# Performance work log

Measured on AMD Instinct MI355X. Metric: run time of the kernel, lower is better.

Reference implementation:

```python
import jax, jax.numpy as jnp
import numpy as np

N = 768        # nodes
F = 64         # invariant (0e) hidden channels
V = 16         # vector (1e) hidden channels
NB = 8         # bessel basis size
HR = 64        # radial MLP hidden
T = 2          # interactions
RO_S = 32      # invariant readout channels
RO_V = 16      # vector readout channels
RMAX = 10.0
AVG = float(N - 1)   # avg_num_neighbors (fully connected)
P = F + V + F + V + V  # tensor-product paths: s*Y0->0e, dot(v,Y1)->0e, s*Y1->1e, v*Y0->1e, cross(v,Y1)->1e


def _edges(n):
    # fully connected neighbor list (cut_off = 1e6, no pbc): all i != j
    s, r = np.meshgrid(np.arange(n), np.arange(n), indexing='ij')
    m = s != r
    return jnp.asarray(s[m]), jnp.asarray(r[m])


def _bessel(r):
    # bessel_basis(number=NB): sqrt(2/r_max) * sin(n*pi*r/r_max) / r
    n = jnp.arange(1, NB + 1, dtype=r.dtype)
    return jnp.sqrt(2.0 / RMAX) * jnp.sin(n * jnp.pi * r[:, None] / RMAX) / r[:, None]


def _envelope(r):
    # soft_envelope: 1.2 * sus(2*(1 - r/r_max)), sus(u) = exp(-1/u) for u>0 else 0
    u = 2.0 * (1.0 - r / RMAX)
    safe = jnp.where(u > 0, u, 1.0)
    return 1.2 * jnp.where(u > 0, jnp.exp(-1.0 / safe), 0.0)


def setup_inputs() -> dict:
    key = jax.random.key(0)
    ks = jax.random.split(key, 12)
    rn = lambda k, shp, fan: jax.random.normal(k, shp, jnp.float32) / np.sqrt(fan)
    return {
        'x': jax.random.normal(ks[0], (N, 3), jnp.float32),
        'embed': rn(ks[1], (1, F), 1),
        'w_node_s': rn(ks[2], (T, F, F), F),
        'w_node_v': rn(ks[3], (T, V, V), V),
        'w_rad1': rn(ks[4], (T, NB, HR), NB),
        'b_rad1': jnp.zeros((T, HR), jnp.float32),
        'w_rad2': rn(ks[5], (T, HR, P), HR),
        'w_mix_s': rn(ks[6], (T, F + V, F), F + V),
        'w_mix_v': rn(ks[7], (T, F + 2 * V, V), F + 2 * V),
        'w_gate': rn(ks[8], (T, F, V), F),
        'w_ro_s': rn(ks[9], (T, F, RO_S), F),
        'w_ro_v': rn(ks[10], (T, V, RO_V), V),
    }


def reference(x, embed, w_node_s, w_node_v, w_rad1, b_rad1, w_rad2,
              w_mix_s, w_mix_v, w_gate, w_ro_s, w_ro_v):
    n = x.shape[0]
    com = jnp.mean(x, axis=-2)                       # [3] centre of mass
    senders, receivers = _edges(n)
    vec = x[receivers] - x[senders]                  # [E,3] edge relative vectors
    r = jnp.linalg.norm(vec, axis=-1)                # [E]
    rhat = vec / r[:, None]                          # Y1 spherical harmonics (l=1)
    rb = _bessel(r)                                  # [E,NB]
    env = _envelope(r)                               # [E]

    h_s = jnp.broadcast_to(embed[0], (n, F))         # species embedding (all species 0)
    h_v = jnp.zeros((n, V, 3), x.dtype)
    out_s = jnp.zeros((n, RO_S), x.dtype)
    out_v = jnp.zeros((n, RO_V, 3), x.dtype)

    for t in range(T):
        # node-wise linear before gather
        hs = h_s @ w_node_s[t]                                    # [N,F]
        hv = jnp.einsum('nvc,vw->nwc', h_v, w_node_v[t])          # [N,V,3]
        es = hs[senders]                                          # [E,F]
        ev = hv[senders]                                          # [E,V,3]
        # per-edge tensor-product path weights from radial MLP, enveloped
        R = jax.nn.silu(rb @ w_rad1[t] + b_rad1[t]) @ w_rad2[t] * env[:, None]  # [E,P]
        r1, r2, r3, r4, r5 = (R[:, :F], R[:, F:F + V], R[:, F + V:2 * F + V],
                              R[:, 2 * F + V:2 * F + 2 * V], R[:, 2 * F + 2 * V:])
        # equivariant tensor products with Y0=1, Y1=rhat
        dot = jnp.einsum('evc,ec->ev', ev, rhat)                  # 1e x 1e -> 0e
        msg_s = jnp.concatenate([es * r1, dot * r2], axis=-1)     # [E,F+V]
        v1 = (es * r3)[:, :, None] * rhat[:, None, :]             # 0e x 1e -> 1e  [E,F,3]
        v2 = ev * r4[:, :, None]                                  # 1e x 0e -> 1e  [E,V,3]
        v3 = jnp.cross(ev, rhat[:, None, :]) * r5[:, :, None]     # 1e x 1e -> 1e  [E,V,3]
        msg_v = jnp.concatenate([v1, v2, v3], axis=1)             # [E,F+2V,3]
        # scatter-aggregate to receivers
        agg_s = jax.ops.segment_sum(msg_s, receivers, num_segments=n) / AVG
        agg_v = jax.ops.segment_sum(msg_v, receivers, num_segments=n) / AVG
        # mix + gated nonlinearity
        m_s = agg_s @ w_mix_s[t]                                  # [N,F]
        m_v = jnp.einsum('npc,pv->nvc', agg_v, w_mix_v[t])        # [N,V,3]
        h_s = jax.nn.silu(m_s)
        gate = jax.nn.sigmoid(m_s @ w_gate[t])                    # [N,V]
        h_v = gate[:, :, None] * m_v
        # readout (summed over interactions)
        out_s = out_s + h_s @ w_ro_s[t]
        out_v = out_v + jnp.einsum('nvc,vk->nkc', h_v, w_ro_v[t])

    return out_s, out_v + com
```

## Files before the change

### kernel.cpp

```cpp
#include <hip/hip_runtime.h>
#include <hip/hip_bf16.h>
#include <math.h>

#define Nn 768
#define Ff 64
#define Vv 16
#define NBb 8
#define HRr 64
#define Pp 176
#define TBL 2048
#define ROWC 192
#define RMAXF 10.0f
#define AVGF 767.0f
#define SCALE 204.8f

#define WS_COM   0
#define WS_ES0   16
#define WS_XP    128
#define WS_HST   4096
#define WS_HVT   53248
#define WS_OS    102400
#define WS_OV    126976
#define WS_AGG   163840
#define WS_TBL   458752
#define AGGSTRIDE 368

__device__ __forceinline__ unsigned short f2bf(float f) {
  unsigned b = __float_as_uint(f);
  return (unsigned short)((b + 0x7fffu + ((b >> 16) & 1u)) >> 16);
}
__device__ __forceinline__ float lp(unsigned u, float f) {
  float a = __uint_as_float(u << 16);
  float b = __uint_as_float(u & 0xffff0000u);
  return fmaf(f, b - a, a);
}

__global__ void k_pre(const float* __restrict__ x, const float* __restrict__ embed,
                      const float* __restrict__ wns, float* __restrict__ ws) {
  int b = blockIdx.x, tid = threadIdx.x;
  if (b == 0) {
    __shared__ float red[256][3];
    float a0 = 0, a1 = 0, a2 = 0;
    for (int n = tid; n < Nn; n += 256) {
      a0 += x[n * 3 + 0]; a1 += x[n * 3 + 1]; a2 += x[n * 3 + 2];
    }
    red[tid][0] = a0; red[tid][1] = a1; red[tid][2] = a2;
    __syncthreads();
    if (tid < 3) {
      float a = 0;
      for (int k = 0; k < 256; ++k) a += red[k][tid];
      ws[WS_COM + tid] = a * (1.0f / Nn);
    }
  } else if (b == 1) {
    for (int n = tid; n < Nn; n += 256) {
      ws[WS_XP + n * 4 + 0] = x[n * 3 + 0];
      ws[WS_XP + n * 4 + 1] = x[n * 3 + 1];
      ws[WS_XP + n * 4 + 2] = x[n * 3 + 2];
      ws[WS_XP + n * 4 + 3] = 0.0f;
    }
  } else {
    if (tid < 64) {
      float a = 0;
      for (int k = 0; k < 64; ++k) a = fmaf(embed[k], wns[k * 64 + tid], a);
      ws[WS_ES0 + tid] = a;
    }
  }
}

__global__ __launch_bounds__(256) void k_table(const float* __restrict__ w1,
                                               const float* __restrict__ b1,
                                               const float* __restrict__ w2,
                                               float* __restrict__ ws, int t) {
  __shared__ float w2s[64][Pp];
  __shared__ float w1s[NBb][64];
  __shared__ float b1s[64];
  __shared__ float hid[9][65];
  const int tid = threadIdx.x;
  const int r0 = blockIdx.x * 8;
  const float* W2 = w2 + t * HRr * Pp;
  for (int k = tid; k < 64 * Pp; k += 256) w2s[k / Pp][k % Pp] = W2[k];
  for (int k = tid; k < NBb * 64; k += 256) w1s[k >> 6][k & 63] = w1[t * NBb * 64 + k];
  if (tid < 64) b1s[tid] = b1[t * 64 + tid];
  __syncthreads();
  {
    int rl4 = tid >> 6, h = tid & 63;
    const float c0 = 0.447213595f;
    const float pif = 3.14159265358979f;
    for (int pass = 0; pass < 3; ++pass) {
      int row_l = pass * 4 + rl4;
      if (row_l < 9) {
        int row = r0 + row_l;
        float r = row * (RMAXF / TBL);
        float acc = b1s[h];
        if (row == 0) {
          for (int n = 0; n < NBb; ++n) acc = fmaf(c0 * (n + 1) * (pif / RMAXF), w1s[n][h], acc);
        } else {
          float inv = 1.0f / r;
          for (int n = 0; n < NBb; ++n)
            acc = fmaf(c0 * sinf((n + 1) * pif * r / RMAXF) * inv, w1s[n][h], acc);
        }
        hid[row_l][h] = acc / (1.0f + expf(-acc));
      }
    }
  }
  __syncthreads();
  unsigned* T = (unsigned*)(ws + WS_TBL);
  const int rl = tid & 7, colg = tid >> 3;
  const int rowa = r0 + rl;
  float ra = rowa * (RMAXF / TBL), rb = (rowa + 1) * (RMAXF / TBL);
  float ua = 2.0f * (1.0f - ra / RMAXF), ub = 2.0f * (1.0f - rb / RMAXF);
  float env_a = (ua > 0.0f) ? 1.2f * expf(-1.0f / ua) : 0.0f;
  float env_b = (ub > 0.0f) ? 1.2f * expf(-1.0f / ub) : 0.0f;
  float accA[6], accB[6];
  int pcol[6]; bool zc[6];
#pragma unroll
  for (int c = 0; c < 6; ++c) {
    int col = colg * 6 + c;
    int p = 0; bool z = false;
    if (col < 64) p = col;
    else if (col < 128) p = 80 + (col - 64);
    else {
      int vv = (col - 128) >> 2, k = (col - 128) & 3;
      if (k == 0) p = 64 + vv; else if (k == 1) p = 144 + vv;
      else if (k == 2) p = 160 + vv; else z = true;
    }
    pcol[c] = p; zc[c] = z; accA[c] = 0.0f; accB[c] = 0.0f;
  }
  for (int h = 0; h < 64; ++h) {
    float ha = hid[rl][h], hb = hid[rl + 1][h];
#pragma unroll
    for (int c = 0; c < 6; ++c) {
      float w = w2s[h][pcol[c]];
      accA[c] = fmaf(ha, w, accA[c]);
      accB[c] = fmaf(hb, w, accB[c]);
    }
  }
#pragma unroll
  for (int c = 0; c < 6; ++c) {
    int col = colg * 6 + c;
    float va = zc[c] ? 0.0f : accA[c] * env_a;
    float vb = zc[c] ? 0.0f : accB[c] * env_b;
    T[rowa * ROWC + col] = ((unsigned)f2bf(vb) << 16) | (unsigned)f2bf(va);
  }
  if (blockIdx.x == 255) {
    for (int k = tid; k < ROWC; k += 256) T[2048 * ROWC + k] = 0u;
  }
}

__global__ __launch_bounds__(256) void k_edge0(float* __restrict__ ws) {
  const int blk = blockIdx.x, i = blk >> 2, part = blk & 3;
  const int tid = threadIdx.x;
  const int w = tid >> 6, lane = tid & 63, sq = (lane >> 4) & 3, idx = lane & 15;
  __shared__ float4 GEO[192];
  __shared__ float wb[4][16][16];
  const float4* XP4 = (const float4*)(ws + WS_XP);
  const uint4* T4 = (const uint4*)(ws + WS_TBL);
  const float4 xi = XP4[i];
  if (tid < 192) {
    int j = part * 192 + tid;
    float4 xj = XP4[j];
    float dx = xi.x - xj.x, dy = xi.y - xj.y, dz = xi.z - xj.z;
    float r2 = dx * dx + dy * dy + dz * dz;
    float u, hx, hy, hz;
    if (j == i || r2 <= 0.0f) { u = 2048.0f; hx = hy = hz = 0.0f; }
    else {
      float rinv = rsqrtf(r2);
      hx = dx * rinv; hy = dy * rinv; hz = dz * rinv;
      u = fminf(r2 * rinv * SCALE, 2048.0f);
    }
    GEO[tid] = make_float4(hx, hy, hz, u);
  }
  __syncthreads();
  float s1[4] = {0, 0, 0, 0};
  float v1[4][3] = {};
  for (int q = 0; q < 12; ++q) {
    int jl = w * 48 + q * 4 + sq;
    float4 g = GEO[jl];
    int i0 = (int)g.w;
    float fr = g.w - (float)i0;
    const uint4* rp = T4 + i0 * 48;
    uint4 t1 = rp[idx];
    uint4 t3 = rp[16 + idx];
    s1[0] += lp(t1.x, fr); s1[1] += lp(t1.y, fr);
    s1[2] += lp(t1.z, fr); s1[3] += lp(t1.w, fr);
    float ax = lp(t3.x, fr), ay = lp(t3.y, fr), az = lp(t3.z, fr), aw = lp(t3.w, fr);
    v1[0][0] += ax * g.x; v1[0][1] += ax * g.y; v1[0][2] += ax * g.z;
    v1[1][0] += ay * g.x; v1[1][1] += ay * g.y; v1[1][2] += ay * g.z;
    v1[2][0] += az * g.x; v1[2][1] += az * g.y; v1[2][2] += az * g.z;
    v1[3][0] += aw * g.x; v1[3][1] += aw * g.y; v1[3][2] += aw * g.z;
  }
  float vals[16] = {s1[0], s1[1], s1[2], s1[3],
                    v1[0][0], v1[0][1], v1[0][2], v1[1][0], v1[1][1], v1[1][2],
                    v1[2][0], v1[2][1], v1[2][2], v1[3][0], v1[3][1], v1[3][2]};
#pragma unroll
  for (int k = 0; k < 16; ++k) {
    float v = vals[k];
    v += __shfl_xor(v, 16);
    v += __shfl_xor(v, 32);
    if (lane < 16) wb[w][lane][k] = v;
  }
  __syncthreads();
  {
    int l, s;
    if (tid < 64) { l = tid >> 2; s = tid & 3; }
    else { int p = tid - 64, f = p / 3, c = p - 3 * f; l = f >> 2; s = 4 + 3 * (f & 3) + c; }
    float a = wb[0][l][s] + wb[1][l][s] + wb[2][l][s] + wb[3][l][s];
    atomicAdd(&ws[WS_AGG + i * AGGSTRIDE + tid], a);
  }
}

__global__ __launch_bounds__(256) void k_edge1(float* __restrict__ ws) {
  const int blk = blockIdx.x, i = blk >> 2, part = blk & 3;
  const int tid = threadIdx.x;
  const int w = tid >> 6, lane = tid & 63, sq = (lane >> 4) & 3, idx = lane & 15;
  __shared__ float4 GEO[192];
  __shared__ float wb[4][16][24];
  const float4* XP4 = (const float4*)(ws + WS_XP);
  const uint4* T4 = (const uint4*)(ws + WS_TBL);
  const float4* HS4 = (const float4*)(ws + WS_HST);
  const float4* HV4 = (const float4*)(ws + WS_HVT);
  const float4 xi = XP4[i];
  if (tid < 192) {
    int j = part * 192 + tid;
    float4 xj = XP4[j];
    float dx = xi.x - xj.x, dy = xi.y - xj.y, dz = xi.z - xj.z;
    float r2 = dx * dx + dy * dy + dz * dz;
    float u, hx, hy, hz;
    if (j == i || r2 <= 0.0f) { u = 2048.0f; hx = hy = hz = 0.0f; }
    else {
      float rinv = rsqrtf(r2);
      hx = dx * rinv; hy = dy * rinv; hz = dz * rinv;
      u = fminf(r2 * rinv * SCALE, 2048.0f);
    }
    GEO[tid] = make_float4(hx, hy, hz, u);
  }
  __syncthreads();
  float s1[4] = {0, 0, 0, 0};
  float v1[4][3] = {};
  float s2 = 0, v2x = 0, v2y = 0, v2z = 0, v3x = 0, v3y = 0, v3z = 0;
  const int jbase = part * 192;
  for (int q = 0; q < 12; ++q) {
    int jl = w * 48 + q * 4 + sq;
    float4 g = GEO[jl];
    int i0 = (int)g.w;
    float fr = g.w - (float)i0;
    const uint4* rp = T4 + i0 * 48;
    uint4 t1 = rp[idx];
    uint4 t3 = rp[16 + idx];
    uint4 tv = rp[32 + idx];
    int jg = jbase + jl;
    float4 es = HS4[jg * 16 + idx];
    float4 ev = HV4[jg * 16 + idx];
    s1[0] += es.x * lp(t1.x, fr); s1[1] += es.y * lp(t1.y, fr);
    s1[2] += es.z * lp(t1.z, fr); s1[3] += es.w * lp(t1.w, fr);
    float ax = es.x * lp(t3.x, fr), ay = es.y * lp(t3.y, fr);
    float az = es.z * lp(t3.z, fr), aw = es.w * lp(t3.w, fr);
    v1[0][0] += ax * g.x; v1[0][1] += ax * g.y; v1[0][2] += ax * g.z;
    v1[1][0] += ay * g.x; v1[1][1] += ay * g.y; v1[1][2] += ay * g.z;
    v1[2][0] += az * g.x; v1[2][1] += az * g.y; v1[2][2] += az * g.z;
    v1[3][0] += aw * g.x; v1[3][1] += aw * g.y; v1[3][2] += aw * g.z;
    float rr2 = lp(tv.x, fr), rr4 = lp(tv.y, fr), rr5 = lp(tv.z, fr);
    float dt = ev.x * g.x + ev.y * g.y + ev.z * g.z;
    s2 += dt * rr2;
    v2x += ev.x * rr4; v2y += ev.y * rr4; v2z += ev.z * rr4;
    v3x += (ev.y * g.z - ev.z * g.y) * rr5;
    v3y += (ev.z * g.x - ev.x * g.z) * rr5;
    v3z += (ev.x * g.y - ev.y * g.x) * rr5;
  }
  float vals[23] = {s1[0], s1[1], s1[2], s1[3],
                    v1[0][0], v1[0][1], v1[0][2], v1[1][0], v1[1][1], v1[1][2],
                    v1[2][0], v1[2][1], v1[2][2], v1[3][0], v1[3][1], v1[3][2],
                    s2, v2x, v2y, v2z, v3x, v3y, v3z};
#pragma unroll
  for (int k = 0; k < 23; ++k) {
    float v = vals[k];
    v += __shfl_xor(v, 16);
    v += __shfl_xor(v, 32);
    if (lane < 16) wb[w][lane][k] = v;
  }
  __syncthreads();
  for (int s = tid; s < 368; s += 256) {
    int l, sl;
    if (s < 64) { l = s >> 2; sl = s & 3; }
    else if (s < 80) { l = s - 64; sl = 16; }
    else if (s < 272) { int p = s - 80, f = p / 3, c = p - 3 * f; l = f >> 2; sl = 4 + 3 * (f & 3) + c; }
    else if (s < 320) { int p = s - 272, v = p / 3, c = p - 3 * v; l = v; sl = 17 + c; }
    else { int p = s - 320, v = p / 3, c = p - 3 * v; l = v; sl = 20 + c; }
    float a = wb[0][l][sl] + wb[1][l][sl] + wb[2][l][sl] + wb[3][l][sl];
    atomicAdd(&ws[WS_AGG + i * AGGSTRIDE + s], a);
  }
}

__global__ __launch_bounds__(256) void k_post(const float* __restrict__ wns,
                                              const float* __restrict__ wnv,
                                              const float* __restrict__ wmixs,
                                              const float* __restrict__ wmixv,
                                              const float* __restrict__ wgate,
                                              const float* __restrict__ wros,
                                              const float* __restrict__ wrov,
                                              float* __restrict__ ws,
                                              float* __restrict__ out, int t) {
  const int i = blockIdx.x, tid = threadIdx.x;
  __shared__ float agg[368];
  __shared__ float ms[64], mvv[16][3], gate[16], hsn[64], hvn[16][4];
  const float inv = 1.0f / AVGF;
  const float* A = ws + WS_AGG + i * AGGSTRIDE;
  if (t == 0) {
    for (int s = tid; s < 368; s += 256) {
      float val;
      if (s < 64) val = ws[WS_ES0 + s] * A[s] * inv;
      else if (s < 80) val = 0.0f;
      else if (s < 272) { int p = s - 80, f = p / 3; val = ws[WS_ES0 + f] * A[64 + p] * inv; }
      else val = 0.0f;
      agg[s] = val;
    }
  } else {
    for (int s = tid; s < 368; s += 256) agg[s] = A[s] * inv;
  }
  __syncthreads();
  if (tid < 64) {
    const float* Wm = wmixs + t * 80 * 64;
    float a = 0;
    for (int p = 0; p < 80; ++p) a = fmaf(agg[p], Wm[p * 64 + tid], a);
    ms[tid] = a;
  } else if (tid < 112) {
    int c = (tid - 64) >> 4, v = (tid - 64) & 15;
    const float* Wv = wmixv + t * 96 * 16;
    float a = 0;
    for (int p = 0; p < 96; ++p) {
      int ai = (p < 64) ? (80 + p * 3 + c) : (p < 80 ? (272 + (p - 64) * 3 + c)
                                                     : (320 + (p - 80) * 3 + c));
      a = fmaf(agg[ai], Wv[p * 16 + v], a);
    }
    mvv[v][c] = a;
  }
  __syncthreads();
  if (tid < 64) {
    float m = ms[tid];
    hsn[tid] = m / (1.0f + expf(-m));
  } else if (tid < 80) {
    int v = tid - 64;
    const float* Wg = wgate + t * 64 * 16;
    float a = 0;
    for (int f = 0; f < 64; ++f) a = fmaf(ms[f], Wg[f * 16 + v], a);
    gate[v] = 1.0f / (1.0f + expf(-a));
  }
  __syncthreads();
  if (tid < 64) {
    int v = tid >> 2, c = tid & 3;
    hvn[v][c] = (c < 3) ? gate[v] * mvv[v][c] : 0.0f;
  }
  __syncthreads();
  if (t == 0) {
    if (tid < 32) {
      float a = 0;
      for (int f = 0; f < 64; ++f) a = fmaf(hsn[f], wros[f * 32 + tid], a);
      ws[WS_OS + i * 32 + tid] = a;
    } else if (tid < 80) {
      int p = tid - 32, k = p / 3, c = p - 3 * k;
      float a = 0;
      for (int v = 0; v < 16; ++v) a = fmaf(hvn[v][c], wrov[v * 16 + k], a);
      ws[WS_OV + i * 48 + p] = a;
    } else if (tid < 144) {
      int f2 = tid - 80;
      const float* Wn = wns + 64 * 64;
      float a = 0;
      for (int f = 0; f < 64; ++f) a = fmaf(hsn[f], Wn[f * 64 + f2], a);
      ws[WS_HST + i * 64 + f2] = a;
    } else if (tid < 208) {
      int s = tid - 144, wv = s >> 2, c = s & 3;
      float a = 0;
      if (c < 3) {
        const float* Wn = wnv + 16 * 16;
        for (int v = 0; v < 16; ++v) a = fmaf(hvn[v][c], Wn[v * 16 + wv], a);
      }
      ws[WS_HVT + i * 64 + s] = a;
    }
  } else {
    if (tid < 32) {
      const float* Wr = wros + 64 * 32;
      float a = ws[WS_OS + i * 32 + tid];
      for (int f = 0; f < 64; ++f) a = fmaf(hsn[f], Wr[f * 32 + tid], a);
      out[i * 32 + tid] = a;
    } else if (tid < 80) {
      int p = tid - 32, k = p / 3, c = p - 3 * k;
      const float* Wr = wrov + 16 * 16;
      float a = ws[WS_OV + i * 48 + p] + ws[WS_COM + c];
      for (int v = 0; v < 16; ++v) a = fmaf(hvn[v][c], Wr[v * 16 + k], a);
      out[Nn * 32 + i * 48 + p] = a;
    }
  }
}

extern "C" void kernel_launch(void* const* d_in, const int* in_sizes, int n_in,
                              void* d_out, int out_size, void* d_ws, size_t ws_size,
                              hipStream_t stream) {
  const float* x     = (const float*)d_in[0];
  const float* embed = (const float*)d_in[1];
  const float* wns   = (const float*)d_in[2];
  const float* wnv   = (const float*)d_in[3];
  const float* w1    = (const float*)d_in[4];
  const float* b1    = (const float*)d_in[5];
  const float* w2    = (const float*)d_in[6];
  const float* wmixs = (const float*)d_in[7];
  const float* wmixv = (const float*)d_in[8];
  const float* wgate = (const float*)d_in[9];
  const float* wros  = (const float*)d_in[10];
  const float* wrov  = (const float*)d_in[11];
  float* ws = (float*)d_ws;
  float* out = (float*)d_out;

  hipMemsetAsync(ws + WS_AGG, 0, Nn * AGGSTRIDE * sizeof(float), stream);
  hipLaunchKernelGGL(k_pre,   dim3(3),      dim3(256), 0, stream, x, embed, wns, ws);
  hipLaunchKernelGGL(k_table, dim3(256),    dim3(256), 0, stream, w1, b1, w2, ws, 0);
  hipLaunchKernelGGL(k_edge0, dim3(Nn * 4), dim3(256), 0, stream, ws);
  hipLaunchKernelGGL(k_post,  dim3(Nn),     dim3(256), 0, stream,
                     wns, wnv, wmixs, wmixv, wgate, wros, wrov, ws, out, 0);
  hipMemsetAsync(ws + WS_AGG, 0, Nn * AGGSTRIDE * sizeof(float), stream);
  hipLaunchKernelGGL(k_table, dim3(256),    dim3(256), 0, stream, w1, b1, w2, ws, 1);
  hipLaunchKernelGGL(k_edge1, dim3(Nn * 4), dim3(256), 0, stream, ws);
  hipLaunchKernelGGL(k_post,  dim3(Nn),     dim3(256), 0, stream,
                     wns, wnv, wmixs, wmixv, wgate, wros, wrov, ws, out, 1);
}
```

Measured before the change: 174.5 us.

## Merge setup kernels, replace atomics with partial slabs, store node features as bf16

Folds k_pre and both radial-table builds into one k_setup launch, with a separate table per interaction. Each edge kernel now writes its four per-part partial sums to dedicated slabs instead of doing atomicAdd into a buffer cleared by memset, so both memsets go away and the post kernels sum the slabs. Post is split into specialised t=0 and t=1 kernels. The t=0 kernel packs next-layer node features as bf16, which halves gather traffic in k_edge1 at some precision cost. Shared-memory reduction buffers are padded to avoid bank conflicts.

```diff
diff --git a/kernel.cpp b/kernel.cpp
--- a/kernel.cpp
+++ b/kernel.cpp
@@ -17,13 +17,13 @@
 #define WS_COM   0
 #define WS_ES0   16
 #define WS_XP    128
-#define WS_HST   4096
-#define WS_HVT   53248
-#define WS_OS    102400
-#define WS_OV    126976
-#define WS_AGG   163840
-#define WS_TBL   458752
-#define AGGSTRIDE 368
+#define WS_HSB   4096
+#define WS_HVB   28672
+#define WS_OS    53248
+#define WS_OV    77824
+#define WS_SLAB0 131072
+#define WS_SLAB1 917504
+#define WS_TBL   2097152
 
 __device__ __forceinline__ unsigned short f2bf(float f) {
   unsigned b = __float_as_uint(f);
@@ -34,49 +34,53 @@
   float b = __uint_as_float(u & 0xffff0000u);
   return fmaf(f, b - a, a);
 }
-
-__global__ void k_pre(const float* __restrict__ x, const float* __restrict__ embed,
-                      const float* __restrict__ wns, float* __restrict__ ws) {
-  int b = blockIdx.x, tid = threadIdx.x;
-  if (b == 0) {
-    __shared__ float red[256][3];
-    float a0 = 0, a1 = 0, a2 = 0;
-    for (int n = tid; n < Nn; n += 256) {
-      a0 += x[n * 3 + 0]; a1 += x[n * 3 + 1]; a2 += x[n * 3 + 2];
-    }
-    red[tid][0] = a0; red[tid][1] = a1; red[tid][2] = a2;
-    __syncthreads();
-    if (tid < 3) {
-      float a = 0;
-      for (int k = 0; k < 256; ++k) a += red[k][tid];
-      ws[WS_COM + tid] = a * (1.0f / Nn);
-    }
-  } else if (b == 1) {
-    for (int n = tid; n < Nn; n += 256) {
-      ws[WS_XP + n * 4 + 0] = x[n * 3 + 0];
-      ws[WS_XP + n * 4 + 1] = x[n * 3 + 1];
-      ws[WS_XP + n * 4 + 2] = x[n * 3 + 2];
-      ws[WS_XP + n * 4 + 3] = 0.0f;
-    }
-  } else {
-    if (tid < 64) {
-      float a = 0;
-      for (int k = 0; k < 64; ++k) a = fmaf(embed[k], wns[k * 64 + tid], a);
-      ws[WS_ES0 + tid] = a;
-    }
-  }
-}
-
-__global__ __launch_bounds__(256) void k_table(const float* __restrict__ w1,
+__device__ __forceinline__ float bl(unsigned u) { return __uint_as_float(u << 16); }
+__device__ __forceinline__ float bh(unsigned u) { return __uint_as_float(u & 0xffff0000u); }
+
+__global__ __launch_bounds__(256) void k_setup(const float* __restrict__ x,
+                                               const float* __restrict__ embed,
+                                               const float* __restrict__ wns,
+                                               const float* __restrict__ w1,
                                                const float* __restrict__ b1,
                                                const float* __restrict__ w2,
-                                               float* __restrict__ ws, int t) {
+                                               float* __restrict__ ws) {
+  const int b = blockIdx.x, tid = threadIdx.x;
+  if (b >= 512) {
+    if (b == 512) {
+      __shared__ float red[256][3];
+      float a0 = 0, a1 = 0, a2 = 0;
+      for (int n = tid; n < Nn; n += 256) {
+        a0 += x[n * 3 + 0]; a1 += x[n * 3 + 1]; a2 += x[n * 3 + 2];
+      }
+      red[tid][0] = a0; red[tid][1] = a1; red[tid][2] = a2;
+      __syncthreads();
+      if (tid < 3) {
+        float a = 0;
+        for (int k = 0; k < 256; ++k) a += red[k][tid];
+        ws[WS_COM + tid] = a * (1.0f / Nn);
+      }
+    } else if (b == 513) {
+      for (int n = tid; n < Nn; n += 256) {
+        ws[WS_XP + n * 4 + 0] = x[n * 3 + 0];
+        ws[WS_XP + n * 4 + 1] = x[n * 3 + 1];
+        ws[WS_XP + n * 4 + 2] = x[n * 3 + 2];
+        ws[WS_XP + n * 4 + 3] = 0.0f;
+      }
+    } else {
+      if (tid < 64) {
+        float a = 0;
+        for (int k = 0; k < 64; ++k) a = fmaf(embed[k], wns[k * 64 + tid], a);
+        ws[WS_ES0 + tid] = a;
+      }
+    }
+    return;
+  }
   __shared__ float w2s[64][Pp];
   __shared__ float w1s[NBb][64];
   __shared__ float b1s[64];
   __shared__ float hid[9][65];
-  const int tid = threadIdx.x;
-  const int r0 = blockIdx.x * 8;
+  const int t = b >> 8;
+  const int r0 = (b & 255) * 8;
   const float* W2 = w2 + t * HRr * Pp;
   for (int k = tid; k < 64 * Pp; k += 256) w2s[k / Pp][k % Pp] = W2[k];
   for (int k = tid; k < NBb * 64; k += 256) w1s[k >> 6][k & 63] = w1[t * NBb * 64 + k];
@@ -104,7 +108,7 @@
     }
   }
   __syncthreads();
-  unsigned* T = (unsigned*)(ws + WS_TBL);
+  unsigned* T = (unsigned*)(ws + WS_TBL) + t * 2049 * ROWC;
   const int rl = tid & 7, colg = tid >> 3;
   const int rowa = r0 + rl;
   float ra = rowa * (RMAXF / TBL), rb = (rowa + 1) * (RMAXF / TBL);
@@ -142,7 +146,7 @@
     float vb = zc[c] ? 0.0f : accB[c] * env_b;
     T[rowa * ROWC + col] = ((unsigned)f2bf(vb) << 16) | (unsigned)f2bf(va);
   }
-  if (blockIdx.x == 255) {
+  if ((b & 255) == 255) {
     for (int k = tid; k < ROWC; k += 256) T[2048 * ROWC + k] = 0u;
   }
 }
@@ -152,7 +156,7 @@
   const int tid = threadIdx.x;
   const int w = tid >> 6, lane = tid & 63, sq = (lane >> 4) & 3, idx = lane & 15;
   __shared__ float4 GEO[192];
-  __shared__ float wb[4][16][16];
+  __shared__ float wb[4][16][17];
   const float4* XP4 = (const float4*)(ws + WS_XP);
   const uint4* T4 = (const uint4*)(ws + WS_TBL);
   const float4 xi = XP4[i];
@@ -205,7 +209,94 @@
     if (tid < 64) { l = tid >> 2; s = tid & 3; }
     else { int p = tid - 64, f = p / 3, c = p - 3 * f; l = f >> 2; s = 4 + 3 * (f & 3) + c; }
     float a = wb[0][l][s] + wb[1][l][s] + wb[2][l][s] + wb[3][l][s];
-    atomicAdd(&ws[WS_AGG + i * AGGSTRIDE + tid], a);
+    ws[WS_SLAB0 + (part * Nn + i) * 256 + tid] = a;
+  }
+}
+
+__global__ __launch_bounds__(256) void k_post0(const float* __restrict__ wns,
+                                               const float* __restrict__ wnv,
+                                               const float* __restrict__ wmixs,
+                                               const float* __restrict__ wmixv,
+                                               const float* __restrict__ wgate,
+                                               const float* __restrict__ wros,
+                                               const float* __restrict__ wrov,
+                                               float* __restrict__ ws) {
+  const int i = blockIdx.x, tid = threadIdx.x;
+  __shared__ float agg[256];
+  __shared__ float ms[64], mvv[16][3], gate[16], hsn[64], hvns[16][4];
+  __shared__ float hs1s[64], hv1s[16][4];
+  const float inv = 1.0f / AVGF;
+  const float* S = ws + WS_SLAB0 + i * 256;
+  {
+    float a = S[tid] + S[Nn * 256 + tid] + S[2 * Nn * 256 + tid] + S[3 * Nn * 256 + tid];
+    float es0f = (tid < 64) ? ws[WS_ES0 + tid] : ws[WS_ES0 + (tid - 64) / 3];
+    agg[tid] = a * inv * es0f;
+  }
+  __syncthreads();
+  if (tid < 64) {
+    const float* Wm = wmixs;
+    float a = 0;
+    for (int p = 0; p < 64; ++p) a = fmaf(agg[p], Wm[p * 64 + tid], a);
+    ms[tid] = a;
+  } else if (tid < 112) {
+    int c = (tid - 64) >> 4, v = (tid - 64) & 15;
+    const float* Wv = wmixv;
+    float a = 0;
+    for (int p = 0; p < 64; ++p) a = fmaf(agg[64 + p * 3 + c], Wv[p * 16 + v], a);
+    mvv[v][c] = a;
+  }
+  __syncthreads();
+  if (tid < 64) {
+    float m = ms[tid];
+    hsn[tid] = m / (1.0f + expf(-m));
+  } else if (tid < 80) {
+    int v = tid - 64;
+    float a = 0;
+    for (int f = 0; f < 64; ++f) a = fmaf(ms[f], wgate[f * 16 + v], a);
+    gate[v] = 1.0f / (1.0f + expf(-a));
+  }
+  __syncthreads();
+  if (tid < 64) {
+    int v = tid >> 2, c = tid & 3;
+    hvns[v][c] = (c < 3) ? gate[v] * mvv[v][c] : 0.0f;
+  }
+  __syncthreads();
+  if (tid < 32) {
+    float a = 0;
+    for (int f = 0; f < 64; ++f) a = fmaf(hsn[f], wros[f * 32 + tid], a);
+    ws[WS_OS + i * 32 + tid] = a;
+  } else if (tid < 80) {
+    int p = tid - 32, k = p / 3, c = p - 3 * k;
+    float a = 0;
+    for (int v = 0; v < 16; ++v) a = fmaf(hvns[v][c], wrov[v * 16 + k], a);
+    ws[WS_OV + i * 48 + p] = a;
+  } else if (tid < 144) {
+    int f2 = tid - 80;
+    const float* Wn = wns + 64 * 64;
+    float a = 0;
+    for (int f = 0; f < 64; ++f) a = fmaf(hsn[f], Wn[f * 64 + f2], a);
+    hs1s[f2] = a;
+  } else if (tid < 208) {
+    int s = tid - 144, wv = s >> 2, c = s & 3;
+    float a = 0;
+    if (c < 3) {
+      const float* Wn = wnv + 16 * 16;
+      for (int v = 0; v < 16; ++v) a = fmaf(hvns[v][c], Wn[v * 16 + wv], a);
+    }
+    hv1s[wv][c] = a;
+  }
+  __syncthreads();
+  if (tid < 16) {
+    uint2* HSB = (uint2*)(ws + WS_HSB);
+    unsigned u0 = (unsigned)f2bf(hs1s[4 * tid + 0]) | ((unsigned)f2bf(hs1s[4 * tid + 1]) << 16);
+    unsigned u1 = (unsigned)f2bf(hs1s[4 * tid + 2]) | ((unsigned)f2bf(hs1s[4 * tid + 3]) << 16);
+    HSB[i * 16 + tid] = make_uint2(u0, u1);
+  } else if (tid < 32) {
+    int v = tid - 16;
+    uint2* HVB = (uint2*)(ws + WS_HVB);
+    unsigned u0 = (unsigned)f2bf(hv1s[v][0]) | ((unsigned)f2bf(hv1s[v][1]) << 16);
+    unsigned u1 = (unsigned)f2bf(hv1s[v][2]);
+    HVB[i * 16 + v] = make_uint2(u0, u1);
   }
 }
 
@@ -214,11 +305,11 @@
   const int tid = threadIdx.x;
   const int w = tid >> 6, lane = tid & 63, sq = (lane >> 4) & 3, idx = lane & 15;
   __shared__ float4 GEO[192];
-  __shared__ float wb[4][16][24];
+  __shared__ float wb[4][16][25];
   const float4* XP4 = (const float4*)(ws + WS_XP);
-  const uint4* T4 = (const uint4*)(ws + WS_TBL);
-  const float4* HS4 = (const float4*)(ws + WS_HST);
-  const float4* HV4 = (const float4*)(ws + WS_HVT);
+  const uint4* T4 = (const uint4*)((unsigned*)(ws + WS_TBL) + 2049 * ROWC);
+  const uint2* HSB = (const uint2*)(ws + WS_HSB);
+  const uint2* HVB = (const uint2*)(ws + WS_HVB);
   const float4 xi = XP4[i];
   if (tid < 192) {
     int j = part * 192 + tid;
@@ -249,23 +340,25 @@
     uint4 t3 = rp[16 + idx];
     uint4 tv = rp[32 + idx];
     int jg = jbase + jl;
-    float4 es = HS4[jg * 16 + idx];
-    float4 ev = HV4[jg * 16 + idx];
-    s1[0] += es.x * lp(t1.x, fr); s1[1] += es.y * lp(t1.y, fr);
-    s1[2] += es.z * lp(t1.z, fr); s1[3] += es.w * lp(t1.w, fr);
-    float ax = es.x * lp(t3.x, fr), ay = es.y * lp(t3.y, fr);
-    float az = es.z * lp(t3.z, fr), aw = es.w * lp(t3.w, fr);
+    uint2 esb = HSB[jg * 16 + idx];
+    uint2 evb = HVB[jg * 16 + idx];
+    float esx = bl(esb.x), esy = bh(esb.x), esz = bl(esb.y), esw = bh(esb.y);
+    float evx = bl(evb.x), evy = bh(evb.x), evz = bl(evb.y);
+    s1[0] += esx * lp(t1.x, fr); s1[1] += esy * lp(t1.y, fr);
+    s1[2] += esz * lp(t1.z, fr); s1[3] += esw * lp(t1.w, fr);
+    float ax = esx * lp(t3.x, fr), ay = esy * lp(t3.y, fr);
+    float az = esz * lp(t3.z, fr), aw = esw * lp(t3.w, fr);
     v1[0][0] += ax * g.x; v1[0][1] += ax * g.y; v1[0][2] += ax * g.z;
     v1[1][0] += ay * g.x; v1[1][1] += ay * g.y; v1[1][2] += ay * g.z;
     v1[2][0] += az * g.x; v1[2][1] += az * g.y; v1[2][2] += az * g.z;
     v1[3][0] += aw * g.x; v1[3][1] += aw * g.y; v1[3][2] += aw * g.z;
     float rr2 = lp(tv.x, fr), rr4 = lp(tv.y, fr), rr5 = lp(tv.z, fr);
-    float dt = ev.x * g.x + ev.y * g.y + ev.z * g.z;
+    float dt = evx * g.x + evy * g.y + evz * g.z;
     s2 += dt * rr2;
-    v2x += ev.x * rr4; v2y += ev.y * rr4; v2z += ev.z * rr4;
-    v3x += (ev.y * g.z - ev.z * g.y) * rr5;
-    v3y += (ev.z * g.x - ev.x * g.z) * rr5;
-    v3z += (ev.x * g.y - ev.y * g.x) * rr5;
+    v2x += evx * rr4; v2y += evy * rr4; v2z += evz * rr4;
+    v3x += (evy * g.z - evz * g.y) * rr5;
+    v3y += (evz * g.x - evx * g.z) * rr5;
+    v3z += (evx * g.y - evy * g.x) * rr5;
   }
   float vals[23] = {s1[0], s1[1], s1[2], s1[3],
                     v1[0][0], v1[0][1], v1[0][2], v1[1][0], v1[1][1], v1[1][2],
@@ -286,46 +379,34 @@
     else if (s < 272) { int p = s - 80, f = p / 3, c = p - 3 * f; l = f >> 2; sl = 4 + 3 * (f & 3) + c; }
     else if (s < 320) { int p = s - 272, v = p / 3, c = p - 3 * v; l = v; sl = 17 + c; }
     else { int p = s - 320, v = p / 3, c = p - 3 * v; l = v; sl = 20 + c; }
-    float a = wb[0][l][sl] + wb[1][l][sl] + wb[2][l][sl] + wb[3][l][sl];
-    atomicAdd(&ws[WS_AGG + i * AGGSTRIDE + s], a);
-  }
-}
-
-__global__ __launch_bounds__(256) void k_post(const float* __restrict__ wns,
-                                              const float* __restrict__ wnv,
-                                              const float* __restrict__ wmixs,
-                                              const float* __restrict__ wmixv,
-                                              const float* __restrict__ wgate,
-                                              const float* __restrict__ wros,
-                                              const float* __restrict__ wrov,
-                                              float* __restrict__ ws,
-                                              float* __restrict__ out, int t) {
+    ws[WS_SLAB1 + (part * Nn + i) * 384 + s] =
+        wb[0][l][sl] + wb[1][l][sl] + wb[2][l][sl] + wb[3][l][sl];
+  }
+}
+
+__global__ __launch_bounds__(256) void k_post1(const float* __restrict__ wmixs,
+                                               const float* __restrict__ wmixv,
+                                               const float* __restrict__ wgate,
+                                               const float* __restrict__ wros,
+                                               const float* __restrict__ wrov,
+                                               float* __restrict__ ws,
+                                               float* __restrict__ out) {
   const int i = blockIdx.x, tid = threadIdx.x;
   __shared__ float agg[368];
-  __shared__ float ms[64], mvv[16][3], gate[16], hsn[64], hvn[16][4];
+  __shared__ float ms[64], mvv[16][3], gate[16], hsn[64], hvns[16][4];
   const float inv = 1.0f / AVGF;
-  const float* A = ws + WS_AGG + i * AGGSTRIDE;
-  if (t == 0) {
-    for (int s = tid; s < 368; s += 256) {
-      float val;
-      if (s < 64) val = ws[WS_ES0 + s] * A[s] * inv;
-      else if (s < 80) val = 0.0f;
-      else if (s < 272) { int p = s - 80, f = p / 3; val = ws[WS_ES0 + f] * A[64 + p] * inv; }
-      else val = 0.0f;
-      agg[s] = val;
-    }
-  } else {
-    for (int s = tid; s < 368; s += 256) agg[s] = A[s] * inv;
-  }
-  __syncthreads();
-  if (tid < 64) {
-    const float* Wm = wmixs + t * 80 * 64;
+  const float* S = ws + WS_SLAB1 + i * 384;
+  for (int s = tid; s < 368; s += 256)
+    agg[s] = (S[s] + S[Nn * 384 + s] + S[2 * Nn * 384 + s] + S[3 * Nn * 384 + s]) * inv;
+  __syncthreads();
+  if (tid < 64) {
+    const float* Wm = wmixs + 80 * 64;
     float a = 0;
     for (int p = 0; p < 80; ++p) a = fmaf(agg[p], Wm[p * 64 + tid], a);
     ms[tid] = a;
   } else if (tid < 112) {
     int c = (tid - 64) >> 4, v = (tid - 64) & 15;
-    const float* Wv = wmixv + t * 96 * 16;
+    const float* Wv = wmixv + 96 * 16;
     float a = 0;
     for (int p = 0; p < 96; ++p) {
       int ai = (p < 64) ? (80 + p * 3 + c) : (p < 80 ? (272 + (p - 64) * 3 + c)
@@ -340,7 +421,7 @@
     hsn[tid] = m / (1.0f + expf(-m));
   } else if (tid < 80) {
     int v = tid - 64;
-    const float* Wg = wgate + t * 64 * 16;
+    const float* Wg = wgate + 64 * 16;
     float a = 0;
     for (int f = 0; f < 64; ++f) a = fmaf(ms[f], Wg[f * 16 + v], a);
     gate[v] = 1.0f / (1.0f + expf(-a));
@@ -348,47 +429,20 @@
   __syncthreads();
   if (tid < 64) {
     int v = tid >> 2, c = tid & 3;
-    hvn[v][c] = (c < 3) ? gate[v] * mvv[v][c] : 0.0f;
-  }
-  __syncthreads();
-  if (t == 0) {
-    if (tid < 32) {
-      float a = 0;
-      for (int f = 0; f < 64; ++f) a = fmaf(hsn[f], wros[f * 32 + tid], a);
-      ws[WS_OS + i * 32 + tid] = a;
-    } else if (tid < 80) {
-      int p = tid - 32, k = p / 3, c = p - 3 * k;
-      float a = 0;
-      for (int v = 0; v < 16; ++v) a = fmaf(hvn[v][c], wrov[v * 16 + k], a);
-      ws[WS_OV + i * 48 + p] = a;
-    } else if (tid < 144) {
-      int f2 = tid - 80;
-      const float* Wn = wns + 64 * 64;
-      float a = 0;
-      for (int f = 0; f < 64; ++f) a = fmaf(hsn[f], Wn[f * 64 + f2], a);
-      ws[WS_HST + i * 64 + f2] = a;
-    } else if (tid < 208) {
-      int s = tid - 144, wv = s >> 2, c = s & 3;
-      float a = 0;
-      if (c < 3) {
-        const float* Wn = wnv + 16 * 16;
-        for (int v = 0; v < 16; ++v) a = fmaf(hvn[v][c], Wn[v * 16 + wv], a);
-      }
-      ws[WS_HVT + i * 64 + s] = a;
-    }
-  } else {
-    if (tid < 32) {
-      const float* Wr = wros + 64 * 32;
-      float a = ws[WS_OS + i * 32 + tid];
-      for (int f = 0; f < 64; ++f) a = fmaf(hsn[f], Wr[f * 32 + tid], a);
-      out[i * 32 + tid] = a;
-    } else if (tid < 80) {
-      int p = tid - 32, k = p / 3, c = p - 3 * k;
-      const float* Wr = wrov + 16 * 16;
-      float a = ws[WS_OV + i * 48 + p] + ws[WS_COM + c];
-      for (int v = 0; v < 16; ++v) a = fmaf(hvn[v][c], Wr[v * 16 + k], a);
-      out[Nn * 32 + i * 48 + p] = a;
-    }
+    hvns[v][c] = (c < 3) ? gate[v] * mvv[v][c] : 0.0f;
+  }
+  __syncthreads();
+  if (tid < 32) {
+    const float* Wr = wros + 64 * 32;
+    float a = ws[WS_OS + i * 32 + tid];
+    for (int f = 0; f < 64; ++f) a = fmaf(hsn[f], Wr[f * 32 + tid], a);
+    out[i * 32 + tid] = a;
+  } else if (tid < 80) {
+    int p = tid - 32, k = p / 3, c = p - 3 * k;
+    const float* Wr = wrov + 16 * 16;
+    float a = ws[WS_OV + i * 48 + p] + ws[WS_COM + c];
+    for (int v = 0; v < 16; ++v) a = fmaf(hvns[v][c], Wr[v * 16 + k], a);
+    out[Nn * 32 + i * 48 + p] = a;
   }
 }
 
@@ -410,15 +464,11 @@
   float* ws = (float*)d_ws;
   float* out = (float*)d_out;
 
-  hipMemsetAsync(ws + WS_AGG, 0, Nn * AGGSTRIDE * sizeof(float), stream);
-  hipLaunchKernelGGL(k_pre,   dim3(3),      dim3(256), 0, stream, x, embed, wns, ws);
-  hipLaunchKernelGGL(k_table, dim3(256),    dim3(256), 0, stream, w1, b1, w2, ws, 0);
+  hipLaunchKernelGGL(k_setup, dim3(515),    dim3(256), 0, stream, x, embed, wns, w1, b1, w2, ws);
   hipLaunchKernelGGL(k_edge0, dim3(Nn * 4), dim3(256), 0, stream, ws);
-  hipLaunchKernelGGL(k_post,  dim3(Nn),     dim3(256), 0, stream,
-                     wns, wnv, wmixs, wmixv, wgate, wros, wrov, ws, out, 0);
-  hipMemsetAsync(ws + WS_AGG, 0, Nn * AGGSTRIDE * sizeof(float), stream);
-  hipLaunchKernelGGL(k_table, dim3(256),    dim3(256), 0, stream, w1, b1, w2, ws, 1);
+  hipLaunchKernelGGL(k_post0, dim3(Nn),     dim3(256), 0, stream,
+                     wns, wnv, wmixs, wmixv, wgate, wros, wrov, ws);
   hipLaunchKernelGGL(k_edge1, dim3(Nn * 4), dim3(256), 0, stream, ws);
-  hipLaunchKernelGGL(k_post,  dim3(Nn),     dim3(256), 0, stream,
-                     wns, wnv, wmixs, wmixv, wgate, wros, wrov, ws, out, 1);
-}
+  hipLaunchKernelGGL(k_post1, dim3(Nn),     dim3(256), 0, stream,
+                     wmixs, wmixv, wgate, wros, wrov, ws, out);
+}
```

New measurement: 155.3 us. -11.0%, faster.
